# Kernel optimization log

Hardware: AMD Instinct MI355X
Metric: run time of the kernel (lower is better)

## Reference

```python
import jax, jax.numpy as jnp
import numpy as np

EOS_COEF = 0.1


def setup_inputs() -> dict:
    key = jax.random.key(0)
    k1, k2, k3, k4 = jax.random.split(key, 4)
    B, Q, T, P, M = 8, 256, 128, 100, 512
    pred_patch_logits = jax.random.normal(k1, (B, Q, 2), dtype=jnp.float32)
    pred_patch_points = jax.random.normal(k2, (B, Q, P, 3), dtype=jnp.float32)
    tgt_points = jax.random.normal(k3, (B, T, M, 3), dtype=jnp.float32)
    src_idx = jax.random.randint(k4, (B, T), 0, Q, dtype=jnp.int64)
    return {
        'pred_patch_logits': pred_patch_logits,
        'pred_patch_points': pred_patch_points,
        'tgt_points': tgt_points,
        'src_idx': src_idx,
    }


def reference(pred_patch_logits, pred_patch_points, tgt_points, src_idx):
    B, Q, C = pred_patch_logits.shape
    T = src_idx.shape[1]
    P = pred_patch_points.shape[2]
    M = tgt_points.shape[2]
    N = B * T  # total matched patches = num_patches
    bidx = jnp.arange(B)[:, None]

    # ---- loss_valid_labels (weighted CE, empty_weight = [1, eos_coef]) ----
    w = jnp.array([1.0, EOS_COEF], dtype=pred_patch_logits.dtype)
    target_classes = jnp.ones((B, Q), jnp.int32).at[bidx, src_idx].set(0)
    logp = jax.nn.log_softmax(pred_patch_logits, axis=-1)          # [B,Q,2]
    nll = -jnp.take_along_axis(logp, target_classes[..., None], axis=-1)[..., 0]
    wt = w[target_classes]
    loss_ce = jnp.sum(nll * wt) / jnp.sum(wt)

    # accuracy@1 on matched queries (targets are all class 0) and overall
    matched_logits = pred_patch_logits[bidx, src_idx]              # [B,T,2]
    acc_valid = 100.0 * jnp.mean((jnp.argmax(matched_logits, -1) == 0).astype(jnp.float32))
    acc_overall = 100.0 * jnp.mean((jnp.argmax(pred_patch_logits, -1) == target_classes).astype(jnp.float32))

    # ---- loss_cardinality (no-grad, logging) ----
    card_pred = jnp.sum((jnp.argmax(pred_patch_logits, -1) != (C - 1)).astype(jnp.float32), axis=1)
    card_err = jnp.mean(jnp.abs(card_pred - jnp.float32(T)))

    # ---- loss_geometry: per-patch squared chamfer, fused over all patches ----
    src = pred_patch_points[bidx, src_idx].reshape(N, P, 3)        # matched preds
    tgt = tgt_points.reshape(N, M, 3)
    # squared pairwise distances [N,P,M] = |a|^2 + |b|^2 - 2 a.b
    d2 = (jnp.sum(src * src, -1)[:, :, None]
          + jnp.sum(tgt * tgt, -1)[:, None, :]
          - 2.0 * jnp.einsum('npd,nmd->npm', src, tgt))
    d2 = jnp.maximum(d2, 0.0)
    per_patch = (jnp.mean(jnp.min(d2, axis=1), axis=-1)
                 + 0.2 * jnp.mean(jnp.min(d2, axis=2), axis=-1)) / 1.2  # [N]
    loss_geometry = jnp.sum(per_patch) / jnp.float32(N)

    return (loss_ce, acc_valid, acc_overall, card_err, loss_geometry)
```

## Files before the change

### kernel.cpp

```cpp
#include <hip/hip_runtime.h>
#include <math.h>

#define Bq 8
#define Qq 256
#define Tt 128
#define Pp 100
#define Mm 512
#define Nn 1024

__device__ __forceinline__ float breduce256(float v, float* red) {
    #pragma unroll
    for (int off = 32; off > 0; off >>= 1) v += __shfl_down(v, off, 64);
    __syncthreads();
    if ((threadIdx.x & 63) == 0) red[threadIdx.x >> 6] = v;
    __syncthreads();
    return red[0] + red[1] + red[2] + red[3];
}

__global__ __launch_bounds__(256) void fused_kernel(
    const float* __restrict__ logits,
    const float* __restrict__ pred_pts,
    const float* __restrict__ tgt_pts,
    const int*   __restrict__ src_idx,
    float*       __restrict__ per_patch,
    unsigned*    __restrict__ done_ctr,
    float*       __restrict__ out)
{
    __shared__ float4   s_tgt[Mm];
    __shared__ float4   s_src[128];
    __shared__ unsigned s_amin[Mm];
    __shared__ unsigned s_bmin[128];
    __shared__ float    red[4];
    __shared__ unsigned s_lastflag;
    const int n   = blockIdx.x;
    const int tid = threadIdx.x;
    const int b   = n >> 7;
    const int q   = src_idx[n];
    const float* sp = pred_pts + (size_t)(b * Qq + q) * (Pp * 3);
    const float* tp = tgt_pts  + (size_t)n * (Mm * 3);

    {
        const float2* tp2 = (const float2*)tp;
        const float2 a = tp2[3*tid], c2 = tp2[3*tid+1], e = tp2[3*tid+2];
        const int m0 = 2*tid, m1 = 2*tid + 1;
        const int p0 = (m0 & ~15) | ((m0 & 15) ^ ((m0 >> 4) & 7));
        const int p1 = (m1 & ~15) | ((m1 & 15) ^ ((m1 >> 4) & 7));
        s_tgt[p0] = make_float4(a.x, a.y, c2.x, 0.f);
        s_tgt[p1] = make_float4(c2.y, e.x, e.y, 0.f);
    }
    if (tid < 50) {
        const float2* sp2 = (const float2*)sp;
        const float2 a = sp2[3*tid], c2 = sp2[3*tid+1], e = sp2[3*tid+2];
        s_src[2*tid]   = make_float4(a.x, a.y, c2.x, 0.f);
        s_src[2*tid+1] = make_float4(c2.y, e.x, e.y, 0.f);
    } else if (tid >= 100 && tid < 128) {
        s_src[tid] = make_float4(5e18f, 5e18f, 5e18f, 0.f);
    }
    *(uint2*)&s_amin[2*tid] = make_uint2(0x7f7fffffu, 0x7f7fffffu);
    if (tid < 128) s_bmin[tid] = 0x7f7fffffu;
    __syncthreads();

    const int g     = tid & 7;
    const int c     = tid >> 3;
    const int mswz  = c & 7;
    const int mbase = c << 4;
    float4 S[16];
    #pragma unroll
    for (int k = 0; k < 16; ++k) S[k] = s_src[16*g + k];
    float mn[16];
    #pragma unroll
    for (int k = 0; k < 16; ++k) mn[k] = 3.4e38f;

    #pragma unroll
    for (int j = 0; j < 16; ++j) {
        const int idx = mbase + (((j + g) & 15) ^ mswz);
        const float4 t = s_tgt[idx];
        float pmA = 3.4e38f, pmB = 3.4e38f, pmC = 3.4e38f, pmD = 3.4e38f;
        #pragma unroll
        for (int k = 0; k < 16; k += 4) {
            float dx, dy, dz, d;
            dx = S[k].x-t.x;   dy = S[k].y-t.y;   dz = S[k].z-t.z;
            d = fmaf(dx,dx,fmaf(dy,dy,dz*dz)); mn[k]   = fminf(mn[k],   d); pmA = fminf(pmA, d);
            dx = S[k+1].x-t.x; dy = S[k+1].y-t.y; dz = S[k+1].z-t.z;
            d = fmaf(dx,dx,fmaf(dy,dy,dz*dz)); mn[k+1] = fminf(mn[k+1], d); pmB = fminf(pmB, d);
            dx = S[k+2].x-t.x; dy = S[k+2].y-t.y; dz = S[k+2].z-t.z;
            d = fmaf(dx,dx,fmaf(dy,dy,dz*dz)); mn[k+2] = fminf(mn[k+2], d); pmC = fminf(pmC, d);
            dx = S[k+3].x-t.x; dy = S[k+3].y-t.y; dz = S[k+3].z-t.z;
            d = fmaf(dx,dx,fmaf(dy,dy,dz*dz)); mn[k+3] = fminf(mn[k+3], d); pmD = fminf(pmD, d);
        }
        const float pm = fminf(fminf(pmA, pmB), fminf(pmC, pmD));
        atomicMin(&s_amin[idx], __float_as_uint(pm));
    }
    #pragma unroll
    for (int k = 0; k < 16; ++k)
        atomicMin(&s_bmin[16*g + k], __float_as_uint(mn[k]));
    __syncthreads();

    float contrib;
    {
        const uint2 u = *(const uint2*)&s_amin[2*tid];
        contrib = (__uint_as_float(u.x) + __uint_as_float(u.y)) * (1.0f / Mm);
    }
    if (tid < Pp) contrib += 0.2f * __uint_as_float(s_bmin[tid]) * (1.0f / Pp);

    const float tot = breduce256(contrib, red);
    if (tid == 0) {
        per_patch[n] = tot * (1.0f / 1.2f);
        __threadfence();
        s_lastflag = (atomicAdd(done_ctr, 1u) == (unsigned)(Nn - 1));
    }
    __syncthreads();
    if (!s_lastflag) return;

    __shared__ unsigned char matched[Bq * Qq];
    __shared__ int s_card[Bq];
    for (int i = tid; i < Bq * Qq; i += 256) matched[i] = 0;
    if (tid < Bq) s_card[tid] = 0;
    __syncthreads();
    for (int i = tid; i < Nn; i += 256) matched[(i >> 7) * Qq + src_idx[i]] = 1;
    __syncthreads();

    float sum_nll = 0.f, sum_wt = 0.f, cnt_ov = 0.f;
    #pragma unroll
    for (int k = 0; k < 8; ++k) {
        const int i = tid + (k << 8);
        const float2 l = ((const float2*)logits)[i];
        const int mt = matched[i];
        const float mx  = fmaxf(l.x, l.y);
        const float lse = mx + logf(expf(l.x - mx) + expf(l.y - mx));
        sum_nll += (mt ? 1.0f : 0.1f) * (lse - (mt ? l.x : l.y));
        sum_wt  += mt ? 1.0f : 0.1f;
        const int pred0 = (l.x >= l.y) ? 1 : 0;
        cnt_ov += (pred0 == mt) ? 1.f : 0.f;
        const unsigned long long bal = __ballot(pred0);
        if ((tid & 63) == 0) atomicAdd(&s_card[k], (int)__popcll(bal));
    }
    float cnt_va = 0.f, gsum = 0.f;
    const volatile float* vpp = per_patch;
    for (int i = tid; i < Nn; i += 256) {
        const float2 l = ((const float2*)logits)[(i >> 7) * Qq + src_idx[i]];
        cnt_va += (l.x >= l.y) ? 1.f : 0.f;
        gsum   += vpp[i];
    }

    const float t_nll = breduce256(sum_nll, red);
    const float t_wt  = breduce256(sum_wt,  red);
    const float t_ov  = breduce256(cnt_ov,  red);
    const float t_va  = breduce256(cnt_va,  red);
    const float t_gs  = breduce256(gsum,    red);

    if (tid == 0) {
        float cerr = 0.f;
        for (int bb = 0; bb < Bq; ++bb) cerr += fabsf((float)s_card[bb] - (float)Tt);
        out[0] = t_nll / t_wt;
        out[1] = 100.f * t_va / (float)Nn;
        out[2] = 100.f * t_ov / (float)(Bq * Qq);
        out[3] = cerr / (float)Bq;
        out[4] = t_gs / (float)Nn;
    }
}

extern "C" void kernel_launch(void* const* d_in, const int* in_sizes, int n_in,
                              void* d_out, int out_size, void* d_ws, size_t ws_size,
                              hipStream_t stream) {
    const float* logits   = (const float*)d_in[0];
    const float* pred_pts = (const float*)d_in[1];
    const float* tgt_pts  = (const float*)d_in[2];
    const int*   src_idx  = (const int*)  d_in[3];
    float* out       = (float*)d_out;
    float* per_patch = (float*)d_ws;
    unsigned* ctr    = (unsigned*)((char*)d_ws + 4096);

    hipMemsetAsync(ctr, 0, sizeof(unsigned), stream);
    fused_kernel<<<Nn, 256, 0, stream>>>(logits, pred_pts, tgt_pts, src_idx,
                                         per_patch, ctr, out);
}
```

Baseline: 103.9 us.

## Retile chamfer inner loop to 8 src points by 32 targets per thread

Changes the per-thread work tile from 16 source points by 16 targets to 8 source points by 32 targets, and drops the XOR swizzle in favour of a rotated target index. It also adds a launch bound of 4 blocks per CU to cap register use. The aim is to cut register pressure and raise occupancy, at the price of twice as many shared-memory atomicMin operations on the target minima per thread and more LDS traffic for targets.

```diff
diff --git a/kernel.cpp b/kernel.cpp
--- a/kernel.cpp
+++ b/kernel.cpp
@@ -17,7 +17,12 @@
     return red[0] + red[1] + red[2] + red[3];
 }
 
-__global__ __launch_bounds__(256) void fused_kernel(
+__device__ __forceinline__ float dist2(float sx, float sy, float sz, float4 t) {
+    const float dx = sx - t.x, dy = sy - t.y, dz = sz - t.z;
+    return fmaf(dx, dx, fmaf(dy, dy, dz * dz));
+}
+
+__global__ __launch_bounds__(256, 4) void fused_kernel(
     const float* __restrict__ logits,
     const float* __restrict__ pred_pts,
     const float* __restrict__ tgt_pts,
@@ -42,11 +47,8 @@
     {
         const float2* tp2 = (const float2*)tp;
         const float2 a = tp2[3*tid], c2 = tp2[3*tid+1], e = tp2[3*tid+2];
-        const int m0 = 2*tid, m1 = 2*tid + 1;
-        const int p0 = (m0 & ~15) | ((m0 & 15) ^ ((m0 >> 4) & 7));
-        const int p1 = (m1 & ~15) | ((m1 & 15) ^ ((m1 >> 4) & 7));
-        s_tgt[p0] = make_float4(a.x, a.y, c2.x, 0.f);
-        s_tgt[p1] = make_float4(c2.y, e.x, e.y, 0.f);
+        s_tgt[2*tid]   = make_float4(a.x, a.y, c2.x, 0.f);
+        s_tgt[2*tid+1] = make_float4(c2.y, e.x, e.y, 0.f);
     }
     if (tid < 50) {
         const float2* sp2 = (const float2*)sp;
@@ -60,40 +62,48 @@
     if (tid < 128) s_bmin[tid] = 0x7f7fffffu;
     __syncthreads();
 
-    const int g     = tid & 7;
-    const int c     = tid >> 3;
-    const int mswz  = c & 7;
-    const int mbase = c << 4;
-    float4 S[16];
-    #pragma unroll
-    for (int k = 0; k < 16; ++k) S[k] = s_src[16*g + k];
-    float mn[16];
-    #pragma unroll
-    for (int k = 0; k < 16; ++k) mn[k] = 3.4e38f;
+    const int g     = tid & 15;
+    const int c     = tid >> 4;
+    const int mbase = c << 5;
+    const int rot   = (g + ((c & 3) << 3)) & 31;
 
-    #pragma unroll
-    for (int j = 0; j < 16; ++j) {
-        const int idx = mbase + (((j + g) & 15) ^ mswz);
-        const float4 t = s_tgt[idx];
-        float pmA = 3.4e38f, pmB = 3.4e38f, pmC = 3.4e38f, pmD = 3.4e38f;
-        #pragma unroll
-        for (int k = 0; k < 16; k += 4) {
-            float dx, dy, dz, d;
-            dx = S[k].x-t.x;   dy = S[k].y-t.y;   dz = S[k].z-t.z;
-            d = fmaf(dx,dx,fmaf(dy,dy,dz*dz)); mn[k]   = fminf(mn[k],   d); pmA = fminf(pmA, d);
-            dx = S[k+1].x-t.x; dy = S[k+1].y-t.y; dz = S[k+1].z-t.z;
-            d = fmaf(dx,dx,fmaf(dy,dy,dz*dz)); mn[k+1] = fminf(mn[k+1], d); pmB = fminf(pmB, d);
-            dx = S[k+2].x-t.x; dy = S[k+2].y-t.y; dz = S[k+2].z-t.z;
-            d = fmaf(dx,dx,fmaf(dy,dy,dz*dz)); mn[k+2] = fminf(mn[k+2], d); pmC = fminf(pmC, d);
-            dx = S[k+3].x-t.x; dy = S[k+3].y-t.y; dz = S[k+3].z-t.z;
-            d = fmaf(dx,dx,fmaf(dy,dy,dz*dz)); mn[k+3] = fminf(mn[k+3], d); pmD = fminf(pmD, d);
-        }
-        const float pm = fminf(fminf(pmA, pmB), fminf(pmC, pmD));
-        atomicMin(&s_amin[idx], __float_as_uint(pm));
+    const float4 q0 = s_src[8*g+0], q1 = s_src[8*g+1], q2 = s_src[8*g+2], q3 = s_src[8*g+3];
+    const float4 q4 = s_src[8*g+4], q5 = s_src[8*g+5], q6 = s_src[8*g+6], q7 = s_src[8*g+7];
+    const float s0x=q0.x, s0y=q0.y, s0z=q0.z;
+    const float s1x=q1.x, s1y=q1.y, s1z=q1.z;
+    const float s2x=q2.x, s2y=q2.y, s2z=q2.z;
+    const float s3x=q3.x, s3y=q3.y, s3z=q3.z;
+    const float s4x=q4.x, s4y=q4.y, s4z=q4.z;
+    const float s5x=q5.x, s5y=q5.y, s5z=q5.z;
+    const float s6x=q6.x, s6y=q6.y, s6z=q6.z;
+    const float s7x=q7.x, s7y=q7.y, s7z=q7.z;
+    float mn0 = 3.4e38f, mn1 = 3.4e38f, mn2 = 3.4e38f, mn3 = 3.4e38f;
+    float mn4 = 3.4e38f, mn5 = 3.4e38f, mn6 = 3.4e38f, mn7 = 3.4e38f;
+
+    #pragma unroll 8
+    for (int j = 0; j < 32; ++j) {
+        const int m = mbase + ((j + rot) & 31);
+        const float4 t = s_tgt[m];
+        const float d0 = dist2(s0x,s0y,s0z,t); mn0 = fminf(mn0,d0);
+        const float d1 = dist2(s1x,s1y,s1z,t); mn1 = fminf(mn1,d1);
+        const float d2 = dist2(s2x,s2y,s2z,t); mn2 = fminf(mn2,d2);
+        const float d3 = dist2(s3x,s3y,s3z,t); mn3 = fminf(mn3,d3);
+        const float d4 = dist2(s4x,s4y,s4z,t); mn4 = fminf(mn4,d4);
+        const float d5 = dist2(s5x,s5y,s5z,t); mn5 = fminf(mn5,d5);
+        const float d6 = dist2(s6x,s6y,s6z,t); mn6 = fminf(mn6,d6);
+        const float d7 = dist2(s7x,s7y,s7z,t); mn7 = fminf(mn7,d7);
+        const float pm = fminf(fminf(fminf(d0,d1), fminf(d2,d3)),
+                               fminf(fminf(d4,d5), fminf(d6,d7)));
+        atomicMin(&s_amin[m], __float_as_uint(pm));
     }
-    #pragma unroll
-    for (int k = 0; k < 16; ++k)
-        atomicMin(&s_bmin[16*g + k], __float_as_uint(mn[k]));
+    atomicMin(&s_bmin[8*g+0], __float_as_uint(mn0));
+    atomicMin(&s_bmin[8*g+1], __float_as_uint(mn1));
+    atomicMin(&s_bmin[8*g+2], __float_as_uint(mn2));
+    atomicMin(&s_bmin[8*g+3], __float_as_uint(mn3));
+    atomicMin(&s_bmin[8*g+4], __float_as_uint(mn4));
+    atomicMin(&s_bmin[8*g+5], __float_as_uint(mn5));
+    atomicMin(&s_bmin[8*g+6], __float_as_uint(mn6));
+    atomicMin(&s_bmin[8*g+7], __float_as_uint(mn7));
     __syncthreads();
 
     float contrib;
```

Result: faster. 101.3 us (-2.5%).

## Remap chamfer work to 4 sources per thread and partial-min source reduction

Applied to the files above, without the earlier changes.

Changes the thread tiling of the pairwise distance loop from 16 sources by 16 targets to 4 sources by 64 targets per thread. Replaces source-side shared atomics with per-group partial minima reduced after the barrier, and drops the target swizzle in favour of a rotated index. This cuts register usage and source-side atomics but quadruples the number of target-side LDS atomicMin operations.

```diff
diff --git a/kernel.cpp b/kernel.cpp
--- a/kernel.cpp
+++ b/kernel.cpp
@@ -29,7 +29,7 @@
     __shared__ float4   s_tgt[Mm];
     __shared__ float4   s_src[128];
     __shared__ unsigned s_amin[Mm];
-    __shared__ unsigned s_bmin[128];
+    __shared__ float    s_bpart[8][128];
     __shared__ float    red[4];
     __shared__ unsigned s_lastflag;
     const int n   = blockIdx.x;
@@ -42,11 +42,8 @@
     {
         const float2* tp2 = (const float2*)tp;
         const float2 a = tp2[3*tid], c2 = tp2[3*tid+1], e = tp2[3*tid+2];
-        const int m0 = 2*tid, m1 = 2*tid + 1;
-        const int p0 = (m0 & ~15) | ((m0 & 15) ^ ((m0 >> 4) & 7));
-        const int p1 = (m1 & ~15) | ((m1 & 15) ^ ((m1 >> 4) & 7));
-        s_tgt[p0] = make_float4(a.x, a.y, c2.x, 0.f);
-        s_tgt[p1] = make_float4(c2.y, e.x, e.y, 0.f);
+        s_tgt[2*tid]   = make_float4(a.x, a.y, c2.x, 0.f);
+        s_tgt[2*tid+1] = make_float4(c2.y, e.x, e.y, 0.f);
     }
     if (tid < 50) {
         const float2* sp2 = (const float2*)sp;
@@ -57,43 +54,35 @@
         s_src[tid] = make_float4(5e18f, 5e18f, 5e18f, 0.f);
     }
     *(uint2*)&s_amin[2*tid] = make_uint2(0x7f7fffffu, 0x7f7fffffu);
-    if (tid < 128) s_bmin[tid] = 0x7f7fffffu;
     __syncthreads();
 
-    const int g     = tid & 7;
-    const int c     = tid >> 3;
-    const int mswz  = c & 7;
-    const int mbase = c << 4;
-    float4 S[16];
-    #pragma unroll
-    for (int k = 0; k < 16; ++k) S[k] = s_src[16*g + k];
-    float mn[16];
-    #pragma unroll
-    for (int k = 0; k < 16; ++k) mn[k] = 3.4e38f;
+    const int g = tid & 31;
+    const int c = tid >> 5;
+    const int mbase = c << 6;
+    const float4 s0 = s_src[4*g+0], s1 = s_src[4*g+1],
+                 s2 = s_src[4*g+2], s3 = s_src[4*g+3];
+    float mn0 = 3.4e38f, mn1 = 3.4e38f, mn2 = 3.4e38f, mn3 = 3.4e38f;
 
-    #pragma unroll
-    for (int j = 0; j < 16; ++j) {
-        const int idx = mbase + (((j + g) & 15) ^ mswz);
-        const float4 t = s_tgt[idx];
-        float pmA = 3.4e38f, pmB = 3.4e38f, pmC = 3.4e38f, pmD = 3.4e38f;
-        #pragma unroll
-        for (int k = 0; k < 16; k += 4) {
-            float dx, dy, dz, d;
-            dx = S[k].x-t.x;   dy = S[k].y-t.y;   dz = S[k].z-t.z;
-            d = fmaf(dx,dx,fmaf(dy,dy,dz*dz)); mn[k]   = fminf(mn[k],   d); pmA = fminf(pmA, d);
-            dx = S[k+1].x-t.x; dy = S[k+1].y-t.y; dz = S[k+1].z-t.z;
-            d = fmaf(dx,dx,fmaf(dy,dy,dz*dz)); mn[k+1] = fminf(mn[k+1], d); pmB = fminf(pmB, d);
-            dx = S[k+2].x-t.x; dy = S[k+2].y-t.y; dz = S[k+2].z-t.z;
-            d = fmaf(dx,dx,fmaf(dy,dy,dz*dz)); mn[k+2] = fminf(mn[k+2], d); pmC = fminf(pmC, d);
-            dx = S[k+3].x-t.x; dy = S[k+3].y-t.y; dz = S[k+3].z-t.z;
-            d = fmaf(dx,dx,fmaf(dy,dy,dz*dz)); mn[k+3] = fminf(mn[k+3], d); pmD = fminf(pmD, d);
-        }
-        const float pm = fminf(fminf(pmA, pmB), fminf(pmC, pmD));
-        atomicMin(&s_amin[idx], __float_as_uint(pm));
+    #pragma unroll 4
+    for (int j = 0; j < 64; ++j) {
+        const int m = mbase + ((j + g) & 63);
+        const float4 t = s_tgt[m];
+        float dx, dy, dz;
+        dx = s0.x - t.x; dy = s0.y - t.y; dz = s0.z - t.z;
+        const float d0 = fmaf(dx, dx, fmaf(dy, dy, dz * dz));
+        dx = s1.x - t.x; dy = s1.y - t.y; dz = s1.z - t.z;
+        const float d1 = fmaf(dx, dx, fmaf(dy, dy, dz * dz));
+        dx = s2.x - t.x; dy = s2.y - t.y; dz = s2.z - t.z;
+        const float d2 = fmaf(dx, dx, fmaf(dy, dy, dz * dz));
+        dx = s3.x - t.x; dy = s3.y - t.y; dz = s3.z - t.z;
+        const float d3 = fmaf(dx, dx, fmaf(dy, dy, dz * dz));
+        mn0 = fminf(mn0, d0); mn1 = fminf(mn1, d1);
+        mn2 = fminf(mn2, d2); mn3 = fminf(mn3, d3);
+        const float pm = fminf(fminf(d0, d1), fminf(d2, d3));
+        atomicMin(&s_amin[m], __float_as_uint(pm));
     }
-    #pragma unroll
-    for (int k = 0; k < 16; ++k)
-        atomicMin(&s_bmin[16*g + k], __float_as_uint(mn[k]));
+
+    *(float4*)&s_bpart[c][4*g] = make_float4(mn0, mn1, mn2, mn3);
     __syncthreads();
 
     float contrib;
@@ -101,7 +90,12 @@
         const uint2 u = *(const uint2*)&s_amin[2*tid];
         contrib = (__uint_as_float(u.x) + __uint_as_float(u.y)) * (1.0f / Mm);
     }
-    if (tid < Pp) contrib += 0.2f * __uint_as_float(s_bmin[tid]) * (1.0f / Pp);
+    if (tid < Pp) {
+        float mn = s_bpart[0][tid];
+        #pragma unroll
+        for (int cc = 1; cc < 8; ++cc) mn = fminf(mn, s_bpart[cc][tid]);
+        contrib += 0.2f * mn * (1.0f / Pp);
+    }
 
     const float tot = breduce256(contrib, red);
     if (tid == 0) {
```

After: 100.3 us. 3.4% less time.
